# Performance work log

Measured on AMD Instinct MI355X. Metric: run time of the kernel, lower is better.

## Reference

```python
import jax, jax.numpy as jnp
from jax import lax
import numpy as np

DIM = 384
HEADS = 8
MLP_HIDDEN = int(DIM * 4.0)
EPS = 1e-5


def layer_norm(x, g, b):
    m = jnp.mean(x, axis=-1, keepdims=True)
    v = jnp.mean((x - m) ** 2, axis=-1, keepdims=True)
    return (x - m) * lax.rsqrt(v + EPS) * g + b


def conv_pos_enc(x, H, W, w, b):
    # x: (B, N, C) -> depthwise 3x3 conv residual, act=Identity (cpe_act=False)
    B, N, C = x.shape
    feat = jnp.transpose(x, (0, 2, 1)).reshape(B, C, H, W)
    feat = lax.conv_general_dilated(
        feat, w, window_strides=(1, 1), padding='SAME',
        feature_group_count=C, dimension_numbers=('NCHW', 'OIHW', 'NCHW'))
    feat = feat + b[None, :, None, None]
    feat = jnp.transpose(feat.reshape(B, C, N), (0, 2, 1))
    return x + feat


def channel_attn(x, qkv_w, proj_w, proj_b):
    B, N, C = x.shape
    h = HEADS
    hd = C // h
    scale = hd ** (-0.5)
    qkv = x @ qkv_w.T                                # (B, N, 3C)
    qkv = qkv.reshape(B, N, 3, h, hd)
    qkv = jnp.transpose(qkv, (2, 0, 3, 1, 4))        # (3, B, h, N, hd)
    q, k, v = qkv[0], qkv[1], qkv[2]
    k = k * scale
    attn = jnp.einsum('bhnd,bhne->bhde', k, v)       # (B, h, hd, hd)
    attn = jax.nn.softmax(attn, axis=-1)
    out = jnp.einsum('bhde,bhne->bhnd', attn, q)     # (B, h, N, hd)
    out = jnp.transpose(out, (0, 2, 1, 3)).reshape(B, N, C)
    return out @ proj_w.T + proj_b


def mlp(x, fc1_w, fc1_b, fc2_w, fc2_b):
    h = jax.nn.gelu(x @ fc1_w.T + fc1_b, approximate=False)
    return h @ fc2_w.T + fc2_b


def setup_inputs() -> dict:
    key = jax.random.key(0)
    ks = jax.random.split(key, 12)
    C, Hd = DIM, MLP_HIDDEN
    s = 0.02
    return {
        'x': jax.random.normal(ks[0], (32, 784, C), dtype=jnp.float32),
        'H': 28,
        'W': 28,
        'cpe0_w': jax.random.normal(ks[1], (C, 1, 3, 3), dtype=jnp.float32) * s,
        'cpe0_b': jnp.zeros((C,), dtype=jnp.float32),
        'cpe1_w': jax.random.normal(ks[2], (C, 1, 3, 3), dtype=jnp.float32) * s,
        'cpe1_b': jnp.zeros((C,), dtype=jnp.float32),
        'norm1_g': jnp.ones((C,), dtype=jnp.float32),
        'norm1_b': jnp.zeros((C,), dtype=jnp.float32),
        'qkv_w': jax.random.normal(ks[3], (3 * C, C), dtype=jnp.float32) * s,
        'proj_w': jax.random.normal(ks[4], (C, C), dtype=jnp.float32) * s,
        'proj_b': jnp.zeros((C,), dtype=jnp.float32),
        'norm2_g': jnp.ones((C,), dtype=jnp.float32),
        'norm2_b': jnp.zeros((C,), dtype=jnp.float32),
        'fc1_w': jax.random.normal(ks[5], (Hd, C), dtype=jnp.float32) * s,
        'fc1_b': jnp.zeros((Hd,), dtype=jnp.float32),
        'fc2_w': jax.random.normal(ks[6], (C, Hd), dtype=jnp.float32) * s,
        'fc2_b': jnp.zeros((C,), dtype=jnp.float32),
    }


def reference(x, H, W, cpe0_w, cpe0_b, cpe1_w, cpe1_b, norm1_g, norm1_b,
              qkv_w, proj_w, proj_b, norm2_g, norm2_b,
              fc1_w, fc1_b, fc2_w, fc2_b):
    x = conv_pos_enc(x, H, W, cpe0_w, cpe0_b)
    cur = layer_norm(x, norm1_g, norm1_b)
    x = x + channel_attn(cur, qkv_w, proj_w, proj_b)
    x = conv_pos_enc(x, H, W, cpe1_w, cpe1_b)
    x = x + mlp(layer_norm(x, norm2_g, norm2_b), fc1_w, fc1_b, fc2_w, fc2_b)
    return x
```

## Files before the change

kernel.cpp:

```cpp
#include <hip/hip_runtime.h>
#include <hip/hip_bf16.h>
#include <math.h>
#include <stdint.h>

#define B_     32
#define HH_    28
#define WW_    28
#define N_     784
#define C_     384
#define M_     25088
#define HEADS_ 8
#define HD_    48
#define HID_   1536

typedef __bf16 bf16;
typedef __attribute__((ext_vector_type(8))) __bf16 bf16x8;
typedef __attribute__((ext_vector_type(4))) __bf16 bf16x4;
typedef __attribute__((ext_vector_type(4))) float f32x4;

__device__ __forceinline__ void gload_lds16(const void* g, void* l) {
    __builtin_amdgcn_global_load_lds(
        (const __attribute__((address_space(1))) unsigned int*)g,
        (__attribute__((address_space(3))) unsigned int*)(uintptr_t)l,
        16, 0, 0);
}

__device__ __forceinline__ float gelu_f(float v) {
    float u = 0.7978845608028654f * v * (1.f + 0.044715f * v * v);
    return __fdividef(v, 1.f + __expf(-2.f * u));
}

__global__ void convert4_kernel(const float* __restrict__ a, int na,
                                const float* __restrict__ b, int nb,
                                const float* __restrict__ c, int nc,
                                const float* __restrict__ d, int nd,
                                bf16* __restrict__ out) {
    int i = blockIdx.x * 256 + threadIdx.x;
    int j = i;
    const float* src;
    if (j < na) src = a + j;
    else { j -= na;
        if (j < nb) src = b + j;
        else { j -= nb;
            if (j < nc) src = c + j;
            else { j -= nc;
                if (j >= nd) return;
                src = d + j; } } }
    out[i] = (bf16)(*src);
}

__global__ void wtrans_kernel(const float* __restrict__ w0, const float* __restrict__ w1,
                              float* __restrict__ wt0, float* __restrict__ wt1) {
    int i = blockIdx.x * 256 + threadIdx.x;
    if (i >= C_ * 9) return;
    int c = i / 9, t = i - c * 9;
    wt0[t * C_ + c] = w0[i];
    wt1[t * C_ + c] = w1[i];
}

__global__ __launch_bounds__(256)
void cpe_ln_kernel(const float* __restrict__ x, const float* __restrict__ wt,
                   const float* __restrict__ bias, float* __restrict__ y,
                   const float* __restrict__ g, const float* __restrict__ beta,
                   bf16* __restrict__ lnout) {
    const int wave = threadIdx.x >> 6, lane = threadIdx.x & 63;
    const int f = blockIdx.x;
    const int row = (f & 7) * 3136 + (f >> 3) * 4 + wave;
    const int b = row / N_;
    const int n = row - b * N_;
    const int py = n / WW_, px = n - py * WW_;

    float acc[6], ctr[6];
    const float* xrow = x + (size_t)row * C_ + lane;
    #pragma unroll
    for (int j = 0; j < 6; j++) {
        acc[j] = bias[lane + j * 64];
        ctr[j] = xrow[j * 64];
    }

    if (py >= 1 && py <= 26 && px >= 1 && px <= 26) {
        const float* p = x + (size_t)(row - WW_ - 1) * C_ + lane;
        float v[9][6];
        #pragma unroll
        for (int t = 0; t < 9; t++) {
            if (t == 4) continue;
            const float* pt = p + ((t / 3) * WW_ + (t % 3)) * C_;
            #pragma unroll
            for (int j = 0; j < 6; j++) v[t][j] = pt[j * 64];
        }
        #pragma unroll
        for (int t = 0; t < 9; t++) {
            #pragma unroll
            for (int j = 0; j < 6; j++) {
                float xv = (t == 4) ? ctr[j] : v[t][j];
                acc[j] += wt[t * C_ + lane + j * 64] * xv;
            }
        }
    } else {
        #pragma unroll
        for (int t = 0; t < 9; t++) {
            int yy = py + t / 3 - 1, xx = px + t % 3 - 1;
            if (yy < 0 || yy >= HH_ || xx < 0 || xx >= WW_) continue;
            const float* pt = x + (size_t)(b * N_ + yy * WW_ + xx) * C_ + lane;
            #pragma unroll
            for (int j = 0; j < 6; j++)
                acc[j] += wt[t * C_ + lane + j * 64] * pt[j * 64];
        }
    }
    #pragma unroll
    for (int j = 0; j < 6; j++) acc[j] += ctr[j];

    float* yrow = y + (size_t)row * C_ + lane;
    #pragma unroll
    for (int j = 0; j < 6; j++) yrow[j * 64] = acc[j];

    float s = 0.f;
    #pragma unroll
    for (int j = 0; j < 6; j++) s += acc[j];
    #pragma unroll
    for (int off = 1; off < 64; off <<= 1) s += __shfl_xor(s, off, 64);
    float mean = s * (1.f / C_);
    float d[6], vs = 0.f;
    #pragma unroll
    for (int j = 0; j < 6; j++) { d[j] = acc[j] - mean; vs += d[j] * d[j]; }
    #pragma unroll
    for (int off = 1; off < 64; off <<= 1) vs += __shfl_xor(vs, off, 64);
    float rstd = rsqrtf(vs * (1.f / C_) + 1e-5f);
    bf16* lrow = lnout + (size_t)row * C_ + lane;
    #pragma unroll
    for (int j = 0; j < 6; j++) {
        int c = lane + j * 64;
        lrow[j * 64] = (bf16)(d[j] * rstd * g[c] + beta[c]);
    }
}

template<bool BIAS, bool GELU, bool RESID, bool OUTBF>
__global__ __launch_bounds__(512, 4)
void gemm_kernel(const bf16* __restrict__ A, const bf16* __restrict__ Wt,
                 const float* __restrict__ bias, const float* __restrict__ resid,
                 void* __restrict__ outp, int M, int N, int K) {
    __shared__ __align__(16) bf16 S[3 * 12288];

    const int nbn = gridDim.x, nbm = gridDim.y;
    const int f = blockIdx.y * nbn + blockIdx.x;
    const int grp = f / (8 * nbn);
    const int rem = f - grp * 8 * nbn;
    const int rows = min(8, nbm - grp * 8);
    const int bm = (grp * 8 + rem % rows) * 256;
    const int bn = (rem / rows) * 128;

    const int t = threadIdx.x;
    const int wave = t >> 6, lane = t & 63;
    const int wm = (wave >> 1) * 64, wn = (wave & 1) * 64;
    const int quad = lane >> 4, r = lane & 15;

    const int ldrow = lane >> 2;
    const int ldcol = ((lane & 3) ^ ((lane >> 3) & 3)) * 8;

    const bf16 *gp0, *gp1, *gp2;
    int lo0, lo1, lo2;
    {
        const int c0 = 3 * wave;
        #define CHUNK(c, p, lo) \
            if ((c) < 16) { p = A + (size_t)(bm + (c) * 16 + ldrow) * K + ldcol; lo = (c) * 512; } \
            else { p = Wt + (size_t)(bn + ((c) - 16) * 16 + ldrow) * K + ldcol; lo = 8192 + ((c) - 16) * 512; }
        CHUNK(c0 + 0, gp0, lo0);
        CHUNK(c0 + 1, gp1, lo1);
        CHUNK(c0 + 2, gp2, lo2);
        #undef CHUNK
    }

    const int nk = K >> 5;

    auto issue = [&](int st) {
        const int sb = (st % 3) * 12288;
        const int kk = st * 32;
        gload_lds16(gp0 + kk, &S[sb + lo0]);
        gload_lds16(gp1 + kk, &S[sb + lo1]);
        gload_lds16(gp2 + kk, &S[sb + lo2]);
    };

    f32x4 acc[4][4] = {};
    issue(0); issue(1);

    const int sq = (quad ^ ((r >> 1) & 3)) * 8;

    for (int s = 0; s < nk; ++s) {
        if (s + 1 < nk) asm volatile("s_waitcnt vmcnt(3)" ::: "memory");
        else            asm volatile("s_waitcnt vmcnt(0)" ::: "memory");
        asm volatile("s_barrier" ::: "memory");
        if (s + 2 < nk) issue(s + 2);

        const bf16* as = &S[(s % 3) * 12288];
        const bf16* bs = as + 8192;
        bf16x8 af[4], bfr[4];
        #pragma unroll
        for (int i = 0; i < 4; i++)
            af[i] = *(const bf16x8*)(&as[(wm + i * 16 + r) * 32 + sq]);
        #pragma unroll
        for (int j = 0; j < 4; j++)
            bfr[j] = *(const bf16x8*)(&bs[(wn + j * 16 + r) * 32 + sq]);
        #pragma unroll
        for (int i = 0; i < 4; i++)
            #pragma unroll
            for (int j = 0; j < 4; j++)
                acc[i][j] = __builtin_amdgcn_mfma_f32_16x16x32_bf16(bfr[j], af[i], acc[i][j], 0, 0, 0);
    }

    #pragma unroll
    for (int j = 0; j < 4; j++) {
        const int n = bn + wn + j * 16 + quad * 4;
        f32x4 bv = {};
        if (BIAS) bv = *(const f32x4*)(&bias[n]);
        #pragma unroll
        for (int i = 0; i < 4; i++) {
            const size_t m = (size_t)(bm + wm + i * 16 + r);
            f32x4 v = acc[i][j];
            if (BIAS) v += bv;
            if (GELU) {
                #pragma unroll
                for (int e = 0; e < 4; e++) v[e] = gelu_f(v[e]);
            }
            if (RESID) v += *(const f32x4*)(&resid[m * N + n]);
            if (OUTBF) {
                bf16x4 ov;
                #pragma unroll
                for (int e = 0; e < 4; e++) ov[e] = (bf16)v[e];
                *(bf16x4*)((bf16*)outp + m * N + n) = ov;
            } else {
                *(f32x4*)((float*)outp + m * N + n) = v;
            }
        }
    }
}

__global__ __launch_bounds__(256)
void attn_fused_kernel(const bf16* __restrict__ qkvb, bf16* __restrict__ outp) {
    __shared__ __align__(16) bf16 stage[4][3872];
    __shared__ float Sred[4][48][49];
    __shared__ __align__(16) bf16 attn_s[48 * 72];

    const int bh = blockIdx.x;
    const int b = bh >> 3, h = bh & 7;
    const int t = threadIdx.x;
    const int wave = t >> 6, lane = t & 63;
    const int quad = lane >> 4, r = lane & 15;
    const int tensor = lane >> 5;
    const int n_local = lane & 31;

    const size_t qkv_base = (size_t)b * N_ * 1152;
    const int toff = 384 + tensor * 384 + h * 48;

    f32x4 acc[3][3] = {};
    bf16* kT = &stage[wave][0];
    bf16* vT = &stage[wave][1936];
    bf16* myT = &stage[wave][tensor * 1936];

    for (int c = wave; c < 25; c += 4) {
        int n0 = c * 32;
        bf16 rowbuf[48];
        if (n0 + n_local < N_) {
            const uint4* src = (const uint4*)(qkvb + qkv_base + (size_t)(n0 + n_local) * 1152 + toff);
            #pragma unroll
            for (int i = 0; i < 6; i++) *(uint4*)(&rowbuf[i * 8]) = src[i];
        } else {
            #pragma unroll
            for (int i = 0; i < 48; i++) rowbuf[i] = (bf16)0.f;
        }
        #pragma unroll
        for (int d = 0; d < 48; d++) myT[d * 40 + n_local] = rowbuf[d];
        bf16x8 af[3], bfv[3];
        #pragma unroll
        for (int i = 0; i < 3; i++) af[i]  = *(const bf16x8*)(&kT[(i * 16 + r) * 40 + quad * 8]);
        #pragma unroll
        for (int j = 0; j < 3; j++) bfv[j] = *(const bf16x8*)(&vT[(j * 16 + r) * 40 + quad * 8]);
        #pragma unroll
        for (int i = 0; i < 3; i++)
            #pragma unroll
            for (int j = 0; j < 3; j++)
                acc[i][j] = __builtin_amdgcn_mfma_f32_16x16x32_bf16(af[i], bfv[j], acc[i][j], 0, 0, 0);
    }

    #pragma unroll
    for (int i = 0; i < 3; i++)
        #pragma unroll
        for (int j = 0; j < 3; j++)
            #pragma unroll
            for (int e = 0; e < 4; e++)
                Sred[wave][i * 16 + quad * 4 + e][j * 16 + r] = acc[i][j][e];
    __syncthreads();

    if (t < 48) {
        float row[48];
        float mx = -1e30f;
        #pragma unroll
        for (int e = 0; e < 48; e++) {
            float s = Sred[0][t][e] + Sred[1][t][e] + Sred[2][t][e] + Sred[3][t][e];
            s *= 0.14433756729740644f;
            row[e] = s;
            mx = fmaxf(mx, s);
        }
        float sum = 0.f;
        #pragma unroll
        for (int e = 0; e < 48; e++) { float ex = __expf(row[e] - mx); row[e] = ex; sum += ex; }
        float inv = 1.f / sum;
        #pragma unroll
        for (int e = 0; e < 48; e++) attn_s[t * 72 + e] = (bf16)(row[e] * inv);
        #pragma unroll
        for (int e = 48; e < 64; e++) attn_s[t * 72 + e] = (bf16)0.f;
    }
    __syncthreads();

    const bf16* qbase = qkvb + qkv_base + h * 48;
    for (int nt = wave; nt < 49; nt += 4) {
        int n0 = nt * 16;
        f32x4 oacc[3] = {};
        #pragma unroll
        for (int kc = 0; kc < 2; kc++) {
            bf16x8 bq = *(const bf16x8*)(qbase + (size_t)(n0 + r) * 1152 + kc * 32 + quad * 8);
            #pragma unroll
            for (int i = 0; i < 3; i++) {
                bf16x8 aa = *(const bf16x8*)(&attn_s[(i * 16 + r) * 72 + kc * 32 + quad * 8]);
                oacc[i] = __builtin_amdgcn_mfma_f32_16x16x32_bf16(aa, bq, oacc[i], 0, 0, 0);
            }
        }
        #pragma unroll
        for (int i = 0; i < 3; i++) {
            bf16x4 ov;
            #pragma unroll
            for (int e = 0; e < 4; e++) ov[e] = (bf16)oacc[i][e];
            *(bf16x4*)(outp + (size_t)(b * N_ + n0 + r) * 384 + h * 48 + i * 16 + quad * 4) = ov;
        }
    }
}

extern "C" void kernel_launch(void* const* d_in, const int* in_sizes, int n_in,
                              void* d_out, int out_size, void* d_ws, size_t ws_size,
                              hipStream_t stream) {
    const float* x      = (const float*)d_in[0];
    const float* cpe0_w = (const float*)d_in[3];
    const float* cpe0_b = (const float*)d_in[4];
    const float* cpe1_w = (const float*)d_in[5];
    const float* cpe1_b = (const float*)d_in[6];
    const float* n1g    = (const float*)d_in[7];
    const float* n1b    = (const float*)d_in[8];
    const float* qkv_w  = (const float*)d_in[9];
    const float* proj_w = (const float*)d_in[10];
    const float* proj_b = (const float*)d_in[11];
    const float* n2g    = (const float*)d_in[12];
    const float* n2b    = (const float*)d_in[13];
    const float* fc1_w  = (const float*)d_in[14];
    const float* fc1_b  = (const float*)d_in[15];
    const float* fc2_w  = (const float*)d_in[16];
    const float* fc2_b  = (const float*)d_in[17];

    char* ws = (char*)d_ws;
    size_t off = 0;
    bf16* cur    = (bf16*)(ws + off); off += (size_t)M_ * C_ * 2;
    bf16* qkvb   = (bf16*)(ws + off);
    float* x3    = (float*)qkvb;
    off += (size_t)M_ * 1152 * 2;
    bf16* hbuf   = (bf16*)(ws + off); off += (size_t)M_ * HID_ * 2;
    bf16* qkv_wb  = (bf16*)(ws + off); off += (size_t)1152 * 384 * 2;
    bf16* proj_wb = (bf16*)(ws + off); off += (size_t)384 * 384 * 2;
    bf16* fc1_wb  = (bf16*)(ws + off); off += (size_t)HID_ * 384 * 2;
    bf16* fc2_wb  = (bf16*)(ws + off); off += (size_t)384 * HID_ * 2;
    float* wt0    = (float*)(ws + off); off += (size_t)C_ * 9 * 4;
    float* wt1    = (float*)(ws + off); off += (size_t)C_ * 9 * 4;
    float* out = (float*)d_out;

    const int na = 442368, nb = 147456, nc = 589824, nd = 589824;
    convert4_kernel<<<(na + nb + nc + nd + 255) / 256, 256, 0, stream>>>(
        qkv_w, na, proj_w, nb, fc1_w, nc, fc2_w, nd, qkv_wb);
    wtrans_kernel<<<(C_ * 9 + 255) / 256, 256, 0, stream>>>(cpe0_w, cpe1_w, wt0, wt1);

    cpe_ln_kernel<<<M_ / 4, 256, 0, stream>>>(x, wt0, cpe0_b, out, n1g, n1b, cur);
    gemm_kernel<false, false, false, true><<<dim3(1152 / 128, M_ / 256), 512, 0, stream>>>(
        cur, qkv_wb, nullptr, nullptr, qkvb, M_, 1152, 384);
    attn_fused_kernel<<<256, 256, 0, stream>>>(qkvb, cur);
    gemm_kernel<true, false, true, false><<<dim3(384 / 128, M_ / 256), 512, 0, stream>>>(
        cur, proj_wb, proj_b, out, out, M_, 384, 384);
    cpe_ln_kernel<<<M_ / 4, 256, 0, stream>>>(out, wt1, cpe1_b, x3, n2g, n2b, cur);
    gemm_kernel<true, true, false, true><<<dim3(HID_ / 128, M_ / 256), 512, 0, stream>>>(
        cur, fc1_wb, fc1_b, nullptr, hbuf, M_, HID_, 384);
    gemm_kernel<true, false, true, false><<<dim3(384 / 128, M_ / 256), 512, 0, stream>>>(
        hbuf, fc2_wb, fc2_b, x3, out, M_, 384, HID_);
}
```

Before: 398.3 us.

## Deepen GEMM K-tile to 64 with split-phase loads and barrier-interleaved MFMA

Doubles the GEMM K-step per pipeline stage from 32 to 64, splitting each tile into two half-phases whose global-to-LDS loads are issued between the LDS fragment reads and the MFMA bursts. It adds s_setprio around the MFMA block and extra barriers so that loads for tile t+2 overlap compute on tile t. LDS use doubles to 144KB per block and the occupancy hint drops from 4 to 2 blocks per CU. The aim is to cut waitcnt and barrier stalls per unit of work, at the cost of fewer resident blocks and more synchronisation points.

```diff
diff --git a/kernel.cpp b/kernel.cpp
--- a/kernel.cpp
+++ b/kernel.cpp
@@ -135,11 +135,11 @@
 }
 
 template<bool BIAS, bool GELU, bool RESID, bool OUTBF>
-__global__ __launch_bounds__(512, 4)
+__global__ __launch_bounds__(512, 2)
 void gemm_kernel(const bf16* __restrict__ A, const bf16* __restrict__ Wt,
                  const float* __restrict__ bias, const float* __restrict__ resid,
                  void* __restrict__ outp, int M, int N, int K) {
-    __shared__ __align__(16) bf16 S[3 * 12288];
+    __shared__ __align__(16) bf16 S[3 * 24576];
 
     const int nbn = gridDim.x, nbm = gridDim.y;
     const int f = blockIdx.y * nbn + blockIdx.x;
@@ -151,72 +151,79 @@
 
     const int t = threadIdx.x;
     const int wave = t >> 6, lane = t & 63;
-    const int wm = (wave >> 1) * 64, wn = (wave & 1) * 64;
+    const int wm = (wave >> 1) * 64;
+    const int wn = (wave & 1) * 64;
     const int quad = lane >> 4, r = lane & 15;
 
-    const int ldrow = lane >> 2;
-    const int ldcol = ((lane & 3) ^ ((lane >> 3) & 3)) * 8;
-
-    const bf16 *gp0, *gp1, *gp2;
-    int lo0, lo1, lo2;
-    {
-        const int c0 = 3 * wave;
-        #define CHUNK(c, p, lo) \
-            if ((c) < 16) { p = A + (size_t)(bm + (c) * 16 + ldrow) * K + ldcol; lo = (c) * 512; } \
-            else { p = Wt + (size_t)(bn + ((c) - 16) * 16 + ldrow) * K + ldcol; lo = 8192 + ((c) - 16) * 512; }
-        CHUNK(c0 + 0, gp0, lo0);
-        CHUNK(c0 + 1, gp1, lo1);
-        CHUNK(c0 + 2, gp2, lo2);
-        #undef CHUNK
-    }
-
-    const int nk = K >> 5;
-
-    auto issue = [&](int st) {
-        const int sb = (st % 3) * 12288;
-        const int kk = st * 32;
-        gload_lds16(gp0 + kk, &S[sb + lo0]);
-        gload_lds16(gp1 + kk, &S[sb + lo1]);
-        gload_lds16(gp2 + kk, &S[sb + lo2]);
+    const int colsw = ((t & 3) ^ ((t >> 3) & 3)) * 8;
+    const int rA = t >> 2;
+    const bf16* sA0 = A  + (size_t)(bm + rA)       * K + colsw;
+    const bf16* sA1 = A  + (size_t)(bm + 128 + rA) * K + colsw;
+    const bf16* sB  = Wt + (size_t)(bn + rA)       * K + colsw;
+    const int t8 = t * 8;
+
+    const int nt = K >> 6;
+
+    auto issue3 = [&](int tl, int ph) {
+        bf16* buf = &S[(tl % 3) * 24576];
+        const size_t ko = (size_t)tl * 64;
+        if (ph == 0) {
+            gload_lds16(sA0 + ko, buf + 0 * 4096 + t8);
+            gload_lds16(sA1 + ko, buf + 1 * 4096 + t8);
+            gload_lds16(sB  + ko, buf + 4 * 4096 + t8);
+        } else {
+            gload_lds16(sA0 + ko + 32, buf + 2 * 4096 + t8);
+            gload_lds16(sA1 + ko + 32, buf + 3 * 4096 + t8);
+            gload_lds16(sB  + ko + 32, buf + 5 * 4096 + t8);
+        }
     };
 
     f32x4 acc[4][4] = {};
-    issue(0); issue(1);
-
-    const int sq = (quad ^ ((r >> 1) & 3)) * 8;
-
-    for (int s = 0; s < nk; ++s) {
-        if (s + 1 < nk) asm volatile("s_waitcnt vmcnt(3)" ::: "memory");
-        else            asm volatile("s_waitcnt vmcnt(0)" ::: "memory");
-        asm volatile("s_barrier" ::: "memory");
-        if (s + 2 < nk) issue(s + 2);
-
-        const bf16* as = &S[(s % 3) * 12288];
-        const bf16* bs = as + 8192;
-        bf16x8 af[4], bfr[4];
-        #pragma unroll
-        for (int i = 0; i < 4; i++)
-            af[i] = *(const bf16x8*)(&as[(wm + i * 16 + r) * 32 + sq]);
-        #pragma unroll
-        for (int j = 0; j < 4; j++)
-            bfr[j] = *(const bf16x8*)(&bs[(wn + j * 16 + r) * 32 + sq]);
-        #pragma unroll
-        for (int i = 0; i < 4; i++)
+
+    issue3(0, 0); issue3(0, 1); issue3(1, 0); issue3(1, 1);
+    asm volatile("s_waitcnt vmcnt(6)" ::: "memory");
+    __builtin_amdgcn_s_barrier();
+
+    const int sq16 = (quad ^ ((r >> 1) & 3)) * 16;
+
+    for (int tl = 0; tl < nt; ++tl) {
+        const char* as = (const char*)&S[(tl % 3) * 24576];
+        const char* bs = as + 32768;
+        #pragma unroll
+        for (int s2 = 0; s2 < 2; ++s2) {
+            bf16x8 af[4], bfr[4];
+            #pragma unroll
+            for (int i = 0; i < 4; i++)
+                af[i] = *(const bf16x8*)(as + s2 * 16384 + (wm + i * 16 + r) * 64 + sq16);
             #pragma unroll
             for (int j = 0; j < 4; j++)
-                acc[i][j] = __builtin_amdgcn_mfma_f32_16x16x32_bf16(bfr[j], af[i], acc[i][j], 0, 0, 0);
-    }
-
-    #pragma unroll
-    for (int j = 0; j < 4; j++) {
-        const int n = bn + wn + j * 16 + quad * 4;
-        f32x4 bv = {};
-        if (BIAS) bv = *(const f32x4*)(&bias[n]);
-        #pragma unroll
-        for (int i = 0; i < 4; i++) {
-            const size_t m = (size_t)(bm + wm + i * 16 + r);
+                bfr[j] = *(const bf16x8*)(bs + s2 * 8192 + (wn + j * 16 + r) * 64 + sq16);
+            if (tl + 2 < nt) issue3(tl + 2, s2);
+            __builtin_amdgcn_s_barrier();
+            asm volatile("s_waitcnt lgkmcnt(0)" ::: "memory");
+            __builtin_amdgcn_s_setprio(1);
+            #pragma unroll
+            for (int i = 0; i < 4; i++)
+                #pragma unroll
+                for (int j = 0; j < 4; j++)
+                    acc[i][j] = __builtin_amdgcn_mfma_f32_16x16x32_bf16(bfr[j], af[i], acc[i][j], 0, 0, 0);
+            __builtin_amdgcn_s_setprio(0);
+            if (s2 == 1) {
+                if (tl + 2 < nt)      asm volatile("s_waitcnt vmcnt(6)" ::: "memory");
+                else if (tl + 1 < nt) asm volatile("s_waitcnt vmcnt(0)" ::: "memory");
+            }
+            __builtin_amdgcn_s_barrier();
+        }
+    }
+
+    #pragma unroll
+    for (int i = 0; i < 4; i++) {
+        const size_t m = (size_t)(bm + wm + i * 16 + r);
+        #pragma unroll
+        for (int j = 0; j < 4; j++) {
+            const int n = bn + wn + j * 16 + quad * 4;
             f32x4 v = acc[i][j];
-            if (BIAS) v += bv;
+            if (BIAS) v += *(const f32x4*)(&bias[n]);
             if (GELU) {
                 #pragma unroll
                 for (int e = 0; e < 4; e++) v[e] = gelu_f(v[e]);
```

Result: slower. 436.0 us (+9.5%).
